# Kernel tuning notes

Measured on AMD Instinct MI355X. Metric: run time of the kernel, lower is better.

The kernel has to match this reference:

```python
import jax, jax.numpy as jnp
import numpy as np

DIM = 1024
RANK = 128
BLOCK = 3
NUM_EXPERTS = 2 ** BLOCK - 1       # key == 2**BLOCK - 1 has no approximator
TOTAL_KEYS = 2 ** BLOCK
B, T = 8, 4096
INIT_STD = 0.01


def setup_inputs() -> dict:
    key = jax.random.key(0)
    k1, k2, k3, k4 = jax.random.split(key, 4)
    x = jax.random.normal(k1, (B, T, DIM), dtype=jnp.float32)
    router_indices = jax.random.randint(k2, (B, T, 1), 0, TOTAL_KEYS, dtype=jnp.int32)
    LRA_mask = jnp.arange(NUM_EXPERTS, dtype=jnp.int32)
    # nn.Linear weight layouts: down [rank, dim], up [dim, rank], stacked over experts
    Wd = jax.random.normal(k3, (NUM_EXPERTS, RANK, DIM), dtype=jnp.float32) * INIT_STD
    Wu = jax.random.normal(k4, (NUM_EXPERTS, DIM, RANK), dtype=jnp.float32) * INIT_STD
    return {"x": x, "router_indices": router_indices, "LRA_mask": LRA_mask, "Wd": Wd, "Wu": Wu}


def reference(x, router_indices, LRA_mask, Wd, Wu):
    # Each token has exactly one router key, so the per-key in-place updates in
    # the torch loop touch disjoint token sets; the result is a single fused
    # residual update: x[t] += Wu[k] @ (Wd[k] @ x[t]) for active keys k.
    full_one = TOTAL_KEYS - 1
    tok = router_indices[..., 0]                                   # [B,T] int
    # which keys are enabled by LRA_mask (out-of-range keys simply never match)
    key_active = jnp.zeros((TOTAL_KEYS,), dtype=bool).at[jnp.clip(LRA_mask, 0, TOTAL_KEYS - 1)].set(True)
    active = key_active[tok] & (tok != full_one)                   # [B,T] bool
    e_idx = jnp.where(tok == full_one, 0, tok)                     # safe expert index
    onehot = jax.nn.one_hot(e_idx, NUM_EXPERTS, dtype=x.dtype) * active[..., None].astype(x.dtype)  # [B,T,E]
    # dense dispatch: compute per-expert down-proj, select via one-hot, up-proj
    down = jnp.einsum("btd,bte,erd->bter", x, onehot, Wd)          # [B,T,E,R] (masked)
    up = jnp.einsum("bter,edr->btd", down, Wu)                     # [B,T,D]
    return x + up
```

## Files before the change

kernel.cpp:

```cpp
#include <hip/hip_runtime.h>
#include <hip/hip_bf16.h>

#define NTOK    32768
#define DIMD    1024
#define RNK     128
#define NEXP    7
#define FULLKEY 7

using f32x4 = __attribute__((ext_vector_type(4))) float;
using s16x8 = __attribute__((ext_vector_type(8))) short;

__device__ __forceinline__ unsigned short f2bf(float f) {
    unsigned u = __float_as_uint(f);
    u += 0x7fffu + ((u >> 16) & 1u);
    return (unsigned short)(u >> 16);
}

__device__ __forceinline__ unsigned lra_bits(const int* __restrict__ mask) {
    unsigned bits = 0u;
#pragma unroll
    for (int i = 0; i < NEXP; ++i) {
        int m = mask[i];
        m = m < 0 ? 0 : (m > 7 ? 7 : m);
        bits |= (1u << m);
    }
    return bits;
}

__global__ void prep_kernel(const float* __restrict__ x, const int* __restrict__ ridx,
                            const int* __restrict__ mask,
                            const float* __restrict__ Wd, const float* __restrict__ Wu,
                            char* __restrict__ WdF, char* __restrict__ WuF,
                            int* __restrict__ counts, int* __restrict__ bucket,
                            float* __restrict__ out) {
    const int b = blockIdx.x;
    const int tid = threadIdx.x;
    if (b < 896) {
        const int id8 = b * 256 + tid;
        const int NE8 = 114688;
        const float* src;
        char* dst;
        if (id8 < NE8) {
            const int e = id8 >> 14, rem = id8 & 16383;
            const int kc = rem >> 9, nn = (rem >> 6) & 7, l = rem & 63;
            const int r = nn * 16 + (l & 15);
            const int k = kc * 32 + (l >> 4) * 8;
            src = Wd + ((size_t)(e * RNK + r)) * DIMD + k;
            dst = WdF + (size_t)id8 * 16;
        } else {
            const int id = id8 - NE8;
            const int e = id >> 14, rem = id & 16383;
            const int dc = rem >> 10, ksn = (rem >> 6) & 15, l = rem & 63;
            const int d = dc * 64 + (ksn & 3) * 16 + (l & 15);
            const int r = (ksn >> 2) * 32 + (l >> 4) * 8;
            src = Wu + ((size_t)(e * DIMD + d)) * RNK + r;
            dst = WuF + (size_t)id * 16;
        }
        const float4 v0 = *reinterpret_cast<const float4*>(src);
        const float4 v1 = *reinterpret_cast<const float4*>(src + 4);
        ushort4 o0, o1;
        o0.x = f2bf(v0.x); o0.y = f2bf(v0.y); o0.z = f2bf(v0.z); o0.w = f2bf(v0.w);
        o1.x = f2bf(v1.x); o1.y = f2bf(v1.y); o1.z = f2bf(v1.z); o1.w = f2bf(v1.w);
        *reinterpret_cast<ushort4*>(dst) = o0;
        *reinterpret_cast<ushort4*>(dst + 8) = o1;
    } else if (b < 1024) {
        __shared__ int lcnt[8];
        __shared__ int lbase[8];
        if (tid < 8) lcnt[tid] = 0;
        __syncthreads();
        const int t = (b - 896) * 256 + tid;
        const unsigned bits = lra_bits(mask);
        const int k = ridx[t];
        const bool act = (k != FULLKEY) && ((bits >> k) & 1u);
        int pos = -1;
        if (act) pos = atomicAdd(&lcnt[k], 1);
        __syncthreads();
        if (tid < 8 && lcnt[tid] > 0) lbase[tid] = atomicAdd(&counts[tid], lcnt[tid]);
        __syncthreads();
        if (act) bucket[k * NTOK + lbase[k] + pos] = t;
    } else {
        unsigned bits = lra_bits(mask);
        for (int t = b - 1024; t < NTOK; t += 2048) {
            int k = ridx[t];
            bool act = (k != FULLKEY) && ((bits >> k) & 1u);
            if (!act) {
                const float4* src = reinterpret_cast<const float4*>(x + (size_t)t * DIMD);
                float4* dst = reinterpret_cast<float4*>(out + (size_t)t * DIMD);
                dst[tid] = src[tid];
            }
        }
    }
}

__launch_bounds__(256)
__global__ void expert_kernel(const float* __restrict__ x,
                              const char* __restrict__ WdF,
                              const char* __restrict__ WuF,
                              const int* __restrict__ counts,
                              const int* __restrict__ bucket,
                              float* __restrict__ out) {
    const int e = blockIdx.y;
    const int n = counts[e];
    const int tid = threadIdx.x;
    const int w = tid >> 6, l = tid & 63, l15 = l & 15, lk = l >> 4;
    const int* bkt = bucket + e * NTOK;

    __shared__ __align__(16) unsigned short tBuf[4][2048];
    char* tb = reinterpret_cast<char*>(tBuf[w]);

    const char* WdE = WdF + (size_t)e * 262144;
    const char* WuE = WuF + (size_t)e * 262144;
    const f32x4 zero = {0.f, 0.f, 0.f, 0.f};

    for (int tile = blockIdx.x; tile * 64 < n; tile += gridDim.x) {
        int idx = tile * 64 + w * 16 + l15;
        if (idx >= n) idx = n - 1;
        const int t = bkt[idx];
        const float* xr = x + (size_t)t * DIMD;
        int t4[4];
#pragma unroll
        for (int j = 0; j < 4; ++j) t4[j] = __shfl(t, lk * 4 + j);

        f32x4 accD[8];
#pragma unroll
        for (int i = 0; i < 8; ++i) accD[i] = zero;

#pragma unroll 2
        for (int kc = 0; kc < 32; ++kc) {
            const float* p = xr + kc * 32 + lk * 8;
            const f32x4 v0 = *reinterpret_cast<const f32x4*>(p);
            const f32x4 v1 = *reinterpret_cast<const f32x4*>(p + 4);
            s16x8 a;
#pragma unroll
            for (int j = 0; j < 4; ++j) {
                a[j]     = (short)f2bf(v0[j]);
                a[4 + j] = (short)f2bf(v1[j]);
            }
            const char* wp = WdE + kc * 8192 + l * 16;
            s16x8 bfr[8];
#pragma unroll
            for (int nn = 0; nn < 8; ++nn)
                bfr[nn] = *reinterpret_cast<const s16x8*>(wp + nn * 1024);
#pragma unroll
            for (int nn = 0; nn < 8; ++nn)
                accD[nn] = __builtin_amdgcn_mfma_f32_16x16x32_bf16(a, bfr[nn], accD[nn], 0, 0, 0);
        }

#pragma unroll
        for (int nn = 0; nn < 8; ++nn) {
#pragma unroll
            for (int j = 0; j < 4; ++j) {
                const int row = lk * 4 + j;
                const int cb2 = (nn * 16 + l15) * 2;
                *reinterpret_cast<unsigned short*>(
                    tb + row * 256 + (cb2 ^ ((row & 7) << 4))) = f2bf(accD[nn][j]);
            }
        }
        s16x8 a2[4];
#pragma unroll
        for (int ks = 0; ks < 4; ++ks)
            a2[ks] = *reinterpret_cast<const s16x8*>(
                tb + l15 * 256 + ((ks * 64 + lk * 16) ^ ((l15 & 7) << 4)));

        for (int dc = 0; dc < 16; ++dc) {
            const char* wq = WuE + dc * 16384 + l * 16;
            s16x8 bfr[16];
#pragma unroll
            for (int i = 0; i < 16; ++i)
                bfr[i] = *reinterpret_cast<const s16x8*>(wq + i * 1024);
            f32x4 accU[4];
#pragma unroll
            for (int i = 0; i < 4; ++i) accU[i] = zero;
#pragma unroll
            for (int ks = 0; ks < 4; ++ks) {
#pragma unroll
                for (int nn = 0; nn < 4; ++nn) {
                    accU[nn] = __builtin_amdgcn_mfma_f32_16x16x32_bf16(
                        a2[ks], bfr[ks * 4 + nn], accU[nn], 0, 0, 0);
                }
            }
#pragma unroll
            for (int nn = 0; nn < 4; ++nn) {
#pragma unroll
                for (int j = 0; j < 4; ++j) {
                    const size_t off = (size_t)t4[j] * DIMD + dc * 64 + nn * 16 + l15;
                    out[off] = x[off] + accU[nn][j];
                }
            }
        }
    }
}

extern "C" void kernel_launch(void* const* d_in, const int* in_sizes, int n_in,
                              void* d_out, int out_size, void* d_ws, size_t ws_size,
                              hipStream_t stream) {
    const float* x  = (const float*)d_in[0];
    const int* ridx = (const int*)d_in[1];
    const int* mask = (const int*)d_in[2];
    const float* Wd = (const float*)d_in[3];
    const float* Wu = (const float*)d_in[4];
    float* out = (float*)d_out;

    char* ws = (char*)d_ws;
    int* counts = (int*)ws;
    int* bucket = (int*)(ws + 256);
    char* WdF = ws + 917760;
    char* WuF = ws + 2752768;

    hipMemsetAsync(counts, 0, 8 * sizeof(int), stream);
    prep_kernel<<<dim3(3072), dim3(256), 0, stream>>>(x, ridx, mask, Wd, Wu, WdF, WuF, counts, bucket, out);
    expert_kernel<<<dim3(68, NEXP), dim3(256), 0, stream>>>(x, WdF, WuF, counts, bucket, out);
}
```

Measured before the change: 98.26 us.

## Split fused expert kernel into split-K down and D-split up kernels

Replaces the single fused expert kernel with two kernels. The down-projection splits the 1024-wide input dimension in half across a grid z-axis and writes bf16 partial results to a workspace buffer. The up-projection sums the two partials and splits the output dimension four ways across blocks. The goal is more parallelism and shorter per-block work, so the per-expert token imbalance and low block count are less of a bottleneck. In exchange it adds a launch, a round trip of the intermediate through global memory, and an extra bf16 rounding of the partial sums.

```diff
diff --git a/kernel.cpp b/kernel.cpp
--- a/kernel.cpp
+++ b/kernel.cpp
@@ -14,6 +14,10 @@
     unsigned u = __float_as_uint(f);
     u += 0x7fffu + ((u >> 16) & 1u);
     return (unsigned short)(u >> 16);
+}
+
+__device__ __forceinline__ float bf2f(unsigned short h) {
+    return __uint_as_float(((unsigned)h) << 16);
 }
 
 __device__ __forceinline__ unsigned lra_bits(const int* __restrict__ mask) {
@@ -93,13 +97,13 @@
 }
 
 __launch_bounds__(256)
-__global__ void expert_kernel(const float* __restrict__ x,
-                              const char* __restrict__ WdF,
-                              const char* __restrict__ WuF,
-                              const int* __restrict__ counts,
-                              const int* __restrict__ bucket,
-                              float* __restrict__ out) {
+__global__ void down_kernel(const float* __restrict__ x,
+                            const char* __restrict__ WdF,
+                            const int* __restrict__ counts,
+                            const int* __restrict__ bucket,
+                            unsigned short* __restrict__ downP) {
     const int e = blockIdx.y;
+    const int h = blockIdx.z;
     const int n = counts[e];
     const int tid = threadIdx.x;
     const int w = tid >> 6, l = tid & 63, l15 = l & 15, lk = l >> 4;
@@ -109,24 +113,21 @@
     char* tb = reinterpret_cast<char*>(tBuf[w]);
 
     const char* WdE = WdF + (size_t)e * 262144;
-    const char* WuE = WuF + (size_t)e * 262144;
     const f32x4 zero = {0.f, 0.f, 0.f, 0.f};
-
-    for (int tile = blockIdx.x; tile * 64 < n; tile += gridDim.x) {
-        int idx = tile * 64 + w * 16 + l15;
+    const int stride = gridDim.x * 4;
+
+    for (int tile = blockIdx.x * 4 + w; tile * 16 < n; tile += stride) {
+        int idx = tile * 16 + l15;
         if (idx >= n) idx = n - 1;
         const int t = bkt[idx];
-        const float* xr = x + (size_t)t * DIMD;
-        int t4[4];
-#pragma unroll
-        for (int j = 0; j < 4; ++j) t4[j] = __shfl(t, lk * 4 + j);
+        const float* xr = x + (size_t)t * DIMD + h * 512;
 
         f32x4 accD[8];
 #pragma unroll
         for (int i = 0; i < 8; ++i) accD[i] = zero;
 
 #pragma unroll 2
-        for (int kc = 0; kc < 32; ++kc) {
+        for (int kc = 0; kc < 16; ++kc) {
             const float* p = xr + kc * 32 + lk * 8;
             const f32x4 v0 = *reinterpret_cast<const f32x4*>(p);
             const f32x4 v1 = *reinterpret_cast<const f32x4*>(p + 4);
@@ -136,7 +137,7 @@
                 a[j]     = (short)f2bf(v0[j]);
                 a[4 + j] = (short)f2bf(v1[j]);
             }
-            const char* wp = WdE + kc * 8192 + l * 16;
+            const char* wp = WdE + (h * 16 + kc) * 8192 + l * 16;
             s16x8 bfr[8];
 #pragma unroll
             for (int nn = 0; nn < 8; ++nn)
@@ -156,27 +157,76 @@
                     tb + row * 256 + (cb2 ^ ((row & 7) << 4))) = f2bf(accD[nn][j]);
             }
         }
+        unsigned short* dp = downP + ((size_t)h * NTOK + t) * RNK + lk * 8;
+#pragma unroll
+        for (int ks = 0; ks < 4; ++ks) {
+            const s16x8 v = *reinterpret_cast<const s16x8*>(
+                tb + l15 * 256 + ((ks * 64 + lk * 16) ^ ((l15 & 7) << 4)));
+            *reinterpret_cast<s16x8*>(dp + ks * 32) = v;
+        }
+    }
+}
+
+__launch_bounds__(256)
+__global__ void up_kernel(const float* __restrict__ x,
+                          const char* __restrict__ WuF,
+                          const unsigned short* __restrict__ downP,
+                          const int* __restrict__ counts,
+                          const int* __restrict__ bucket,
+                          float* __restrict__ out) {
+    const int e = blockIdx.y;
+    const int g = blockIdx.z;
+    const int n = counts[e];
+    const int tid = threadIdx.x;
+    const int w = tid >> 6, l = tid & 63, l15 = l & 15, lk = l >> 4;
+    const int* bkt = bucket + e * NTOK;
+
+    const char* WuE = WuF + (size_t)e * 262144;
+    const f32x4 zero = {0.f, 0.f, 0.f, 0.f};
+    const int stride = gridDim.x * 4;
+
+    for (int tile = blockIdx.x * 4 + w; tile * 16 < n; tile += stride) {
+        int idx = tile * 16 + l15;
+        if (idx >= n) idx = n - 1;
+        const int t = bkt[idx];
+        int t4[4];
+#pragma unroll
+        for (int j = 0; j < 4; ++j) t4[j] = __shfl(t, lk * 4 + j);
+
+        const unsigned short* dp0 = downP + (size_t)t * RNK + lk * 8;
+        const unsigned short* dp1 = dp0 + (size_t)NTOK * RNK;
         s16x8 a2[4];
 #pragma unroll
-        for (int ks = 0; ks < 4; ++ks)
-            a2[ks] = *reinterpret_cast<const s16x8*>(
-                tb + l15 * 256 + ((ks * 64 + lk * 16) ^ ((l15 & 7) << 4)));
-
-        for (int dc = 0; dc < 16; ++dc) {
+        for (int ks = 0; ks < 4; ++ks) {
+            const s16x8 p0 = *reinterpret_cast<const s16x8*>(dp0 + ks * 32);
+            const s16x8 p1 = *reinterpret_cast<const s16x8*>(dp1 + ks * 32);
+            s16x8 av;
+#pragma unroll
+            for (int j = 0; j < 8; ++j)
+                av[j] = (short)f2bf(bf2f((unsigned short)p0[j]) + bf2f((unsigned short)p1[j]));
+            a2[ks] = av;
+        }
+
+#pragma unroll
+        for (int q = 0; q < 4; ++q) {
+            const int dc = g * 4 + q;
             const char* wq = WuE + dc * 16384 + l * 16;
-            s16x8 bfr[16];
-#pragma unroll
-            for (int i = 0; i < 16; ++i)
-                bfr[i] = *reinterpret_cast<const s16x8*>(wq + i * 1024);
             f32x4 accU[4];
 #pragma unroll
             for (int i = 0; i < 4; ++i) accU[i] = zero;
 #pragma unroll
-            for (int ks = 0; ks < 4; ++ks) {
-#pragma unroll
-                for (int nn = 0; nn < 4; ++nn) {
-                    accU[nn] = __builtin_amdgcn_mfma_f32_16x16x32_bf16(
-                        a2[ks], bfr[ks * 4 + nn], accU[nn], 0, 0, 0);
+            for (int hb = 0; hb < 2; ++hb) {
+                s16x8 bfr[8];
+#pragma unroll
+                for (int i = 0; i < 8; ++i)
+                    bfr[i] = *reinterpret_cast<const s16x8*>(wq + (hb * 8 + i) * 1024);
+#pragma unroll
+                for (int ks = 0; ks < 2; ++ks) {
+#pragma unroll
+                    for (int nn = 0; nn < 4; ++nn) {
+                        accU[nn] = __builtin_amdgcn_mfma_f32_16x16x32_bf16(
+                            a2[hb * 2 + ks], bfr[ks * 4 + nn], accU[nn], 0, 0, 0);
+                    }
                 }
             }
 #pragma unroll
@@ -206,8 +256,10 @@
     int* bucket = (int*)(ws + 256);
     char* WdF = ws + 917760;
     char* WuF = ws + 2752768;
+    unsigned short* downP = (unsigned short*)(ws + 4587776);
 
     hipMemsetAsync(counts, 0, 8 * sizeof(int), stream);
     prep_kernel<<<dim3(3072), dim3(256), 0, stream>>>(x, ridx, mask, Wd, Wu, WdF, WuF, counts, bucket, out);
-    expert_kernel<<<dim3(68, NEXP), dim3(256), 0, stream>>>(x, WdF, WuF, counts, bucket, out);
-}
+    down_kernel<<<dim3(64, NEXP, 2), dim3(256), 0, stream>>>(x, WdF, counts, bucket, downP);
+    up_kernel<<<dim3(64, NEXP, 4), dim3(256), 0, stream>>>(x, WuF, downP, counts, bucket, out);
+}
```

After: 138.8 us. +41.2%, slower.

## Process two 16-token subtiles per wave to reuse expert weight fragments

Applied to the files above, without the earlier changes.

Each wave now handles 32 tokens (two 16-row MFMA subtiles) per iteration instead of 16, so every weight fragment loaded from global memory feeds two MFMAs in both the down- and up-projection. The grid is halved to 34 blocks per expert to match the doubled per-block tile. This targets weight-load bandwidth and latency per MFMA, at the cost of doubled accumulator registers, possibly lower occupancy, and fewer blocks to hide memory latency.

```diff
diff --git a/kernel.cpp b/kernel.cpp
--- a/kernel.cpp
+++ b/kernel.cpp
@@ -112,29 +112,40 @@
     const char* WuE = WuF + (size_t)e * 262144;
     const f32x4 zero = {0.f, 0.f, 0.f, 0.f};
 
-    for (int tile = blockIdx.x; tile * 64 < n; tile += gridDim.x) {
-        int idx = tile * 64 + w * 16 + l15;
-        if (idx >= n) idx = n - 1;
-        const int t = bkt[idx];
-        const float* xr = x + (size_t)t * DIMD;
-        int t4[4];
-#pragma unroll
-        for (int j = 0; j < 4; ++j) t4[j] = __shfl(t, lk * 4 + j);
-
-        f32x4 accD[8];
-#pragma unroll
-        for (int i = 0; i < 8; ++i) accD[i] = zero;
+    for (int it = blockIdx.x; it * 128 < n; it += gridDim.x) {
+        const int base = it * 128 + w * 32;
+        int idxA = base + l15;       if (idxA >= n) idxA = n - 1;
+        int idxB = base + 16 + l15;  if (idxB >= n) idxB = n - 1;
+        const int tA = bkt[idxA];
+        const int tB = bkt[idxB];
+        const float* xrA = x + (size_t)tA * DIMD;
+        const float* xrB = x + (size_t)tB * DIMD;
+        int t4A[4], t4B[4];
+#pragma unroll
+        for (int j = 0; j < 4; ++j) {
+            t4A[j] = __shfl(tA, lk * 4 + j);
+            t4B[j] = __shfl(tB, lk * 4 + j);
+        }
+
+        f32x4 accDA[8], accDB[8];
+#pragma unroll
+        for (int i = 0; i < 8; ++i) { accDA[i] = zero; accDB[i] = zero; }
 
 #pragma unroll 2
         for (int kc = 0; kc < 32; ++kc) {
-            const float* p = xr + kc * 32 + lk * 8;
-            const f32x4 v0 = *reinterpret_cast<const f32x4*>(p);
-            const f32x4 v1 = *reinterpret_cast<const f32x4*>(p + 4);
-            s16x8 a;
+            const float* pA = xrA + kc * 32 + lk * 8;
+            const float* pB = xrB + kc * 32 + lk * 8;
+            const f32x4 vA0 = *reinterpret_cast<const f32x4*>(pA);
+            const f32x4 vA1 = *reinterpret_cast<const f32x4*>(pA + 4);
+            const f32x4 vB0 = *reinterpret_cast<const f32x4*>(pB);
+            const f32x4 vB1 = *reinterpret_cast<const f32x4*>(pB + 4);
+            s16x8 aA, aB;
 #pragma unroll
             for (int j = 0; j < 4; ++j) {
-                a[j]     = (short)f2bf(v0[j]);
-                a[4 + j] = (short)f2bf(v1[j]);
+                aA[j]     = (short)f2bf(vA0[j]);
+                aA[4 + j] = (short)f2bf(vA1[j]);
+                aB[j]     = (short)f2bf(vB0[j]);
+                aB[4 + j] = (short)f2bf(vB1[j]);
             }
             const char* wp = WdE + kc * 8192 + l * 16;
             s16x8 bfr[8];
@@ -142,10 +153,13 @@
             for (int nn = 0; nn < 8; ++nn)
                 bfr[nn] = *reinterpret_cast<const s16x8*>(wp + nn * 1024);
 #pragma unroll
-            for (int nn = 0; nn < 8; ++nn)
-                accD[nn] = __builtin_amdgcn_mfma_f32_16x16x32_bf16(a, bfr[nn], accD[nn], 0, 0, 0);
-        }
-
+            for (int nn = 0; nn < 8; ++nn) {
+                accDA[nn] = __builtin_amdgcn_mfma_f32_16x16x32_bf16(aA, bfr[nn], accDA[nn], 0, 0, 0);
+                accDB[nn] = __builtin_amdgcn_mfma_f32_16x16x32_bf16(aB, bfr[nn], accDB[nn], 0, 0, 0);
+            }
+        }
+
+        s16x8 a2A[4], a2B[4];
 #pragma unroll
         for (int nn = 0; nn < 8; ++nn) {
 #pragma unroll
@@ -153,38 +167,56 @@
                 const int row = lk * 4 + j;
                 const int cb2 = (nn * 16 + l15) * 2;
                 *reinterpret_cast<unsigned short*>(
-                    tb + row * 256 + (cb2 ^ ((row & 7) << 4))) = f2bf(accD[nn][j]);
-            }
-        }
-        s16x8 a2[4];
+                    tb + row * 256 + (cb2 ^ ((row & 7) << 4))) = f2bf(accDA[nn][j]);
+            }
+        }
 #pragma unroll
         for (int ks = 0; ks < 4; ++ks)
-            a2[ks] = *reinterpret_cast<const s16x8*>(
+            a2A[ks] = *reinterpret_cast<const s16x8*>(
                 tb + l15 * 256 + ((ks * 64 + lk * 16) ^ ((l15 & 7) << 4)));
-
+#pragma unroll
+        for (int nn = 0; nn < 8; ++nn) {
+#pragma unroll
+            for (int j = 0; j < 4; ++j) {
+                const int row = lk * 4 + j;
+                const int cb2 = (nn * 16 + l15) * 2;
+                *reinterpret_cast<unsigned short*>(
+                    tb + row * 256 + (cb2 ^ ((row & 7) << 4))) = f2bf(accDB[nn][j]);
+            }
+        }
+#pragma unroll
+        for (int ks = 0; ks < 4; ++ks)
+            a2B[ks] = *reinterpret_cast<const s16x8*>(
+                tb + l15 * 256 + ((ks * 64 + lk * 16) ^ ((l15 & 7) << 4)));
+
+#pragma unroll 2
         for (int dc = 0; dc < 16; ++dc) {
             const char* wq = WuE + dc * 16384 + l * 16;
             s16x8 bfr[16];
 #pragma unroll
             for (int i = 0; i < 16; ++i)
                 bfr[i] = *reinterpret_cast<const s16x8*>(wq + i * 1024);
-            f32x4 accU[4];
-#pragma unroll
-            for (int i = 0; i < 4; ++i) accU[i] = zero;
+            f32x4 accUA[4], accUB[4];
+#pragma unroll
+            for (int i = 0; i < 4; ++i) { accUA[i] = zero; accUB[i] = zero; }
 #pragma unroll
             for (int ks = 0; ks < 4; ++ks) {
 #pragma unroll
                 for (int nn = 0; nn < 4; ++nn) {
-                    accU[nn] = __builtin_amdgcn_mfma_f32_16x16x32_bf16(
-                        a2[ks], bfr[ks * 4 + nn], accU[nn], 0, 0, 0);
+                    accUA[nn] = __builtin_amdgcn_mfma_f32_16x16x32_bf16(
+                        a2A[ks], bfr[ks * 4 + nn], accUA[nn], 0, 0, 0);
+                    accUB[nn] = __builtin_amdgcn_mfma_f32_16x16x32_bf16(
+                        a2B[ks], bfr[ks * 4 + nn], accUB[nn], 0, 0, 0);
                 }
             }
 #pragma unroll
             for (int nn = 0; nn < 4; ++nn) {
 #pragma unroll
                 for (int j = 0; j < 4; ++j) {
-                    const size_t off = (size_t)t4[j] * DIMD + dc * 64 + nn * 16 + l15;
-                    out[off] = x[off] + accU[nn][j];
+                    const size_t offA = (size_t)t4A[j] * DIMD + dc * 64 + nn * 16 + l15;
+                    const size_t offB = (size_t)t4B[j] * DIMD + dc * 64 + nn * 16 + l15;
+                    out[offA] = x[offA] + accUA[nn][j];
+                    out[offB] = x[offB] + accUB[nn][j];
                 }
             }
         }
@@ -209,5 +241,5 @@
 
     hipMemsetAsync(counts, 0, 8 * sizeof(int), stream);
     prep_kernel<<<dim3(3072), dim3(256), 0, stream>>>(x, ridx, mask, Wd, Wu, WdF, WuF, counts, bucket, out);
-    expert_kernel<<<dim3(68, NEXP), dim3(256), 0, stream>>>(x, WdF, WuF, counts, bucket, out);
-}
+    expert_kernel<<<dim3(34, NEXP), dim3(256), 0, stream>>>(x, WdF, WuF, counts, bucket, out);
+}
```

New measurement: 176.3 us. 1.79x slower.
